# Performance work log

Hardware: AMD Instinct MI355X
Metric: run time of the kernel (lower is better)

Reference implementation:

```python
import jax, jax.numpy as jnp
import numpy as np

IN_DIM = 128
HID = 128
OUT_DIM = 16
DICT_LEN = 400000
N_GATES = 4


def setup_inputs() -> dict:
    key = jax.random.key(0)
    ks = jax.random.split(key, 13)
    s = 0.05  # small init scale (stand-in for orthogonal init)
    return {
        "x_t": jax.random.normal(ks[0], (1, 1, IN_DIM), jnp.float32),
        "h": jax.random.normal(ks[1], (1, 1, HID), jnp.float32) * 0.1,
        "c": jax.random.normal(ks[2], (1, 1, HID), jnp.float32) * 0.1,
        "W_i2h": jax.random.normal(ks[3], ((N_GATES + 1) * HID, IN_DIM), jnp.float32) * s,
        "b_i2h": jnp.zeros(((N_GATES + 1) * HID,), jnp.float32),
        "W_h2h": jax.random.normal(ks[4], ((N_GATES + 1) * HID, HID), jnp.float32) * s,
        "b_h2h": jnp.zeros(((N_GATES + 1) * HID,), jnp.float32),
        "mem_keys": jax.random.normal(ks[5], (DICT_LEN, IN_DIM), jnp.float32),
        "mem_vals": jax.random.normal(ks[6], (DICT_LEN, HID), jnp.float32),
        "W_actor": jax.random.normal(ks[7], (OUT_DIM, HID), jnp.float32) * s,
        "b_actor": jnp.zeros((OUT_DIM,), jnp.float32),
        "W_critic": jax.random.normal(ks[8], (1, HID), jnp.float32) * s,
        "b_critic": jnp.zeros((1,), jnp.float32),
    }


def reference(x_t, h, c, W_i2h, b_i2h, W_h2h, b_h2h, mem_keys, mem_vals,
              W_actor, b_actor, W_critic, b_critic):
    # flatten [1, B, D] -> [B, D] (B == 1)
    x = x_t.reshape(x_t.shape[1], -1)
    hh = h.reshape(h.shape[1], -1)
    cc = c.reshape(c.shape[1], -1)
    hd = hh.shape[-1]

    # fused gate preactivation: i2h(x) + h2h(h), shape [1, 5*H]
    preact = x @ W_i2h.T + b_i2h + hh @ W_h2h.T + b_h2h
    gates = jax.nn.sigmoid(preact[:, :N_GATES * hd])
    f_t = gates[:, :hd]
    i_t = gates[:, hd:2 * hd]
    o_t = gates[:, 2 * hd:3 * hd]
    r_t = gates[:, 3 * hd:4 * hd]
    c_new = jnp.tanh(preact[:, N_GATES * hd:])
    c_t = f_t * cc + i_t * c_new

    # DND read: l2-kernel similarity over all stored keys, softmax-weighted value sum
    d2 = jnp.sum((mem_keys - x) ** 2, axis=-1)          # [L]
    sim = -jnp.sqrt(d2 + 1e-6)                           # F.pairwise_distance eps
    w = jax.nn.softmax(sim)                              # [L]
    m_t = jnp.tanh(w @ mem_vals)[None, :]                # [1, H]

    c_t = c_t + r_t * m_t
    h_t = o_t * jnp.tanh(c_t)

    # A2C heads
    pi = jax.nn.softmax(h_t @ W_actor.T + b_actor, axis=-1)  # [1, OUT]
    v = h_t @ W_critic.T + b_critic                          # [1, 1]

    # DND write: append (key=x_t, val=c_t), drop oldest (fixed-capacity dict)
    keys_new = jnp.concatenate([x, mem_keys[:-1]], axis=0)
    vals_new = jnp.concatenate([c_t, mem_vals[:-1]], axis=0)

    out = jnp.concatenate([pi.ravel(), v.ravel(), h_t.ravel(), c_t.ravel()])
    return out, keys_new, vals_new
```

## Files before the change

kernel.cpp:

```cpp
#include <hip/hip_runtime.h>
#include <hip/hip_bf16.h>
#include <math.h>

#define DICT 400000
#define D 128
#define NPAIR (DICT / 2)
#define G1 1024
#define KEYS_OFF 273
#define VALS_OFF (273 + DICT * D)
#define SHIFT 16.0f

typedef float vfloat4 __attribute__((ext_vector_type(4)));

__global__ __launch_bounds__(256) void k_pre(const float* __restrict__ Wi,
                                             const float* __restrict__ bi,
                                             const float* __restrict__ Wh,
                                             const float* __restrict__ bh,
                                             const float* __restrict__ x,
                                             const float* __restrict__ h,
                                             float* __restrict__ pre) {
    const int lane = threadIdx.x & 63;
    const int row = blockIdx.x * 4 + (threadIdx.x >> 6);
    if (row >= 640) return;
    float2 xv = reinterpret_cast<const float2*>(x)[lane];
    float2 hv = reinterpret_cast<const float2*>(h)[lane];
    float2 wi = reinterpret_cast<const float2*>(Wi + row * D)[lane];
    float2 wh = reinterpret_cast<const float2*>(Wh + row * D)[lane];
    float dot = wi.x * xv.x + wi.y * xv.y + wh.x * hv.x + wh.y * hv.y;
#pragma unroll
    for (int off = 32; off; off >>= 1) dot += __shfl_xor(dot, off);
    if (lane == 0) pre[row] = dot + bi[row] + bh[row];
}

__device__ __forceinline__ void store_window(float* __restrict__ dstK,
                                             float* __restrict__ dstV,
                                             vfloat4 kv, vfloat4 vv,
                                             vfloat4 ek, vfloat4 ev,
                                             int lane, int idx3, int idx4,
                                             int p, bool last) {
    vfloat4 ks, vs;
    float s;
    s = (lane < 3) ? ek.w : kv.w;  ks.x = __shfl(s, idx3);
    s = (lane < 4) ? ek.x : kv.x;  ks.y = __shfl(s, idx4);
    s = (lane < 4) ? ek.y : kv.y;  ks.z = __shfl(s, idx4);
    s = (lane < 4) ? ek.z : kv.z;  ks.w = __shfl(s, idx4);
    s = (lane < 3) ? ev.w : vv.w;  vs.x = __shfl(s, idx3);
    s = (lane < 4) ? ev.x : vv.x;  vs.y = __shfl(s, idx4);
    s = (lane < 4) ? ev.y : vv.y;  vs.z = __shfl(s, idx4);
    s = (lane < 4) ? ev.z : vv.z;  vs.w = __shfl(s, idx4);
    size_t base = (size_t)(2 * p + 1) * 128 + 15 + 4 * (size_t)lane;
    if (!last) {
        *reinterpret_cast<vfloat4*>(dstK + base) = ks;
        *reinterpret_cast<vfloat4*>(dstV + base) = vs;
    } else {
        if (lane < 28) {
            *reinterpret_cast<vfloat4*>(dstK + base) = ks;
            *reinterpret_cast<vfloat4*>(dstV + base) = vs;
        } else if (lane == 28) {
            dstK[base] = ks.x;
            dstV[base] = vs.x;
        }
    }
}

__global__ __launch_bounds__(256) void k_dict(const float* __restrict__ keys,
                                              const float* __restrict__ vals,
                                              const float* __restrict__ x,
                                              float* __restrict__ keys_new,
                                              float* __restrict__ vals_new,
                                              float* __restrict__ partials) {
    const int tid = threadIdx.x;
    const int lane = tid & 63;
    const int half = lane >> 5;
    const int hl = lane & 31;
    const int wv = tid >> 6;
    const int idx3 = (lane + 3) & 63;
    const int idx4 = (lane + 4) & 63;
    const int wave = (blockIdx.x * blockDim.x + tid) >> 6;
    const int nw = (gridDim.x * blockDim.x) >> 6;
    const float4 xv = reinterpret_cast<const float4*>(x)[hl];

    vfloat4 acc = (vfloat4)(0.f);
    float den = 0.f;

#define COMPUTE(kv, vv)                                                             \
    {                                                                               \
        float dx = kv.x - xv.x, dy = kv.y - xv.y, dz = kv.z - xv.z, dw = kv.w - xv.w; \
        float d2 = dx * dx + dy * dy + dz * dz + dw * dw;                           \
        _Pragma("unroll")                                                           \
        for (int off = 16; off; off >>= 1) d2 += __shfl_xor(d2, off);               \
        float e = __expf(SHIFT - sqrtf(d2 + 1e-6f));                                \
        acc.x += e * vv.x; acc.y += e * vv.y;                                       \
        acc.z += e * vv.z; acc.w += e * vv.w;                                       \
        den += e;                                                                   \
    }

    for (int pp = 2 * wave; pp < NPAIR; pp += 2 * nw) {
        const int row0 = 2 * pp + half;
        const int row1 = row0 + 2;
        vfloat4 kv0 = reinterpret_cast<const vfloat4*>(keys + (size_t)row0 * D)[hl];
        vfloat4 kv1 = reinterpret_cast<const vfloat4*>(keys + (size_t)row1 * D)[hl];
        vfloat4 vv0 = reinterpret_cast<const vfloat4*>(vals + (size_t)row0 * D)[hl];
        vfloat4 vv1 = reinterpret_cast<const vfloat4*>(vals + (size_t)row1 * D)[hl];
        vfloat4 ek1 = (vfloat4)(0.f), ev1 = (vfloat4)(0.f);
        if (lane < 4) {
            const int erow = min(2 * pp + 4, DICT - 1);
            ek1 = *reinterpret_cast<const vfloat4*>(keys + (size_t)erow * D + 4 * lane);
            ev1 = *reinterpret_cast<const vfloat4*>(vals + (size_t)erow * D + 4 * lane);
        }

        COMPUTE(kv0, vv0)
        COMPUTE(kv1, vv1)

        if (pp == 0 && lane < 15) {
            keys_new[128 + lane] = keys[lane];
            vals_new[128 + lane] = vals[lane];
        }
        store_window(keys_new, vals_new, kv0, vv0, kv1, vv1, lane, idx3, idx4,
                     pp, false);
        store_window(keys_new, vals_new, kv1, vv1, ek1, ev1, lane, idx3, idx4,
                     pp + 1, pp + 1 == NPAIR - 1);
    }
#undef COMPUTE

    acc.x += __shfl_xor(acc.x, 32);
    acc.y += __shfl_xor(acc.y, 32);
    acc.z += __shfl_xor(acc.z, 32);
    acc.w += __shfl_xor(acc.w, 32);
    den += __shfl_xor(den, 32);

    __shared__ float lnum[4][128];
    __shared__ float lden[4];
    if (lane < 32) {
        lnum[wv][hl * 4 + 0] = acc.x;
        lnum[wv][hl * 4 + 1] = acc.y;
        lnum[wv][hl * 4 + 2] = acc.z;
        lnum[wv][hl * 4 + 3] = acc.w;
    }
    if (lane == 0) lden[wv] = den;
    __syncthreads();
    if (tid < 128) {
        float s = lnum[0][tid] + lnum[1][tid] + lnum[2][tid] + lnum[3][tid];
        partials[(size_t)tid * G1 + blockIdx.x] = s;
    } else if (tid == 128) {
        partials[(size_t)128 * G1 + blockIdx.x] = lden[0] + lden[1] + lden[2] + lden[3];
    }
}

__global__ __launch_bounds__(256) void k_red(const float* __restrict__ partials,
                                             float* __restrict__ red) {
    const int j = blockIdx.x;
    float s = 0.f;
    for (int b = threadIdx.x; b < G1; b += 256) s += partials[(size_t)j * G1 + b];
#pragma unroll
    for (int off = 32; off; off >>= 1) s += __shfl_xor(s, off);
    __shared__ float w4[4];
    if ((threadIdx.x & 63) == 0) w4[threadIdx.x >> 6] = s;
    __syncthreads();
    if (threadIdx.x == 0) red[j] = w4[0] + w4[1] + w4[2] + w4[3];
}

__global__ __launch_bounds__(256) void k_tail(const float* __restrict__ red,
                                              const float* __restrict__ pre,
                                              const float* __restrict__ x,
                                              const float* __restrict__ c,
                                              const float* __restrict__ Wa,
                                              const float* __restrict__ ba,
                                              const float* __restrict__ Wc,
                                              const float* __restrict__ bc,
                                              float* __restrict__ out) {
    __shared__ float sh_h[128];
    __shared__ float sh_logit[16];
    const int tid = threadIdx.x;
    if (tid < 128) {
        float den = red[128];
        float m = tanhf(red[tid] / den);
        float f  = 1.f / (1.f + __expf(-pre[tid]));
        float i_ = 1.f / (1.f + __expf(-pre[128 + tid]));
        float o  = 1.f / (1.f + __expf(-pre[256 + tid]));
        float r  = 1.f / (1.f + __expf(-pre[384 + tid]));
        float cn = tanhf(pre[512 + tid]);
        float ct = f * c[tid] + i_ * cn + r * m;
        float ht = o * tanhf(ct);
        sh_h[tid] = ht;
        out[17 + tid] = ht;
        out[145 + tid] = ct;
        out[KEYS_OFF + tid] = x[tid];
        out[VALS_OFF + tid] = ct;
    }
    __syncthreads();
    if (tid < 16) {
        float l = ba[tid];
        for (int j = 0; j < 128; ++j) l += Wa[tid * D + j] * sh_h[j];
        sh_logit[tid] = l;
    } else if (tid == 16) {
        float v = bc[0];
        for (int j = 0; j < 128; ++j) v += Wc[j] * sh_h[j];
        out[16] = v;
    }
    __syncthreads();
    if (tid == 0) {
        float mx = sh_logit[0];
        for (int k = 1; k < 16; ++k) mx = fmaxf(mx, sh_logit[k]);
        float e[16];
        float s = 0.f;
        for (int k = 0; k < 16; ++k) { e[k] = __expf(sh_logit[k] - mx); s += e[k]; }
        for (int k = 0; k < 16; ++k) out[k] = e[k] / s;
    }
}

extern "C" void kernel_launch(void* const* d_in, const int* in_sizes, int n_in,
                              void* d_out, int out_size, void* d_ws, size_t ws_size,
                              hipStream_t stream) {
    const float* x    = (const float*)d_in[0];
    const float* h    = (const float*)d_in[1];
    const float* c    = (const float*)d_in[2];
    const float* Wi   = (const float*)d_in[3];
    const float* bi   = (const float*)d_in[4];
    const float* Wh   = (const float*)d_in[5];
    const float* bh   = (const float*)d_in[6];
    const float* keys = (const float*)d_in[7];
    const float* vals = (const float*)d_in[8];
    const float* Wa   = (const float*)d_in[9];
    const float* ba   = (const float*)d_in[10];
    const float* Wc   = (const float*)d_in[11];
    const float* bc   = (const float*)d_in[12];
    float* out = (float*)d_out;

    char* ws = (char*)d_ws;
    float* red      = (float*)(ws + 0);
    float* pre      = (float*)(ws + 1024);
    float* partials = (float*)(ws + 4096);

    k_pre<<<160, 256, 0, stream>>>(Wi, bi, Wh, bh, x, h, pre);
    k_dict<<<G1, 256, 0, stream>>>(keys, vals, x, out + KEYS_OFF, out + VALS_OFF, partials);
    k_red<<<129, 256, 0, stream>>>(partials, red);
    k_tail<<<1, 256, 0, stream>>>(red, pre, x, c, Wa, ba, Wc, bc, out);
}
```

Baseline: 183.4 us.

## Split dict pass into key-distance phase and value-accumulate phase via LDS weights

The single fused loop over the dictionary is split into two passes. The first streams keys, computes the softmax weights, stores them in shared memory and writes the shifted keys. The second streams values, reads the cached weights, accumulates the weighted sum and writes the shifted values. This removes the serial dependency where value loads waited behind the distance reduction and cuts register pressure per loop. It relies on each wave doing at most 26 iterations, since the shared weight buffer holds 104 entries per wave, and loop-index bookkeeping is duplicated across the two passes.

```diff
diff --git a/kernel.cpp b/kernel.cpp
--- a/kernel.cpp
+++ b/kernel.cpp
@@ -32,34 +32,22 @@
     if (lane == 0) pre[row] = dot + bi[row] + bh[row];
 }
 
-__device__ __forceinline__ void store_window(float* __restrict__ dstK,
-                                             float* __restrict__ dstV,
-                                             vfloat4 kv, vfloat4 vv,
-                                             vfloat4 ek, vfloat4 ev,
-                                             int lane, int idx3, int idx4,
-                                             int p, bool last) {
-    vfloat4 ks, vs;
+__device__ __forceinline__ void store_window1(float* __restrict__ dst,
+                                              vfloat4 kv, vfloat4 ek,
+                                              int lane, int idx3, int idx4,
+                                              int p, bool last) {
+    vfloat4 ks;
     float s;
     s = (lane < 3) ? ek.w : kv.w;  ks.x = __shfl(s, idx3);
     s = (lane < 4) ? ek.x : kv.x;  ks.y = __shfl(s, idx4);
     s = (lane < 4) ? ek.y : kv.y;  ks.z = __shfl(s, idx4);
     s = (lane < 4) ? ek.z : kv.z;  ks.w = __shfl(s, idx4);
-    s = (lane < 3) ? ev.w : vv.w;  vs.x = __shfl(s, idx3);
-    s = (lane < 4) ? ev.x : vv.x;  vs.y = __shfl(s, idx4);
-    s = (lane < 4) ? ev.y : vv.y;  vs.z = __shfl(s, idx4);
-    s = (lane < 4) ? ev.z : vv.z;  vs.w = __shfl(s, idx4);
     size_t base = (size_t)(2 * p + 1) * 128 + 15 + 4 * (size_t)lane;
     if (!last) {
-        *reinterpret_cast<vfloat4*>(dstK + base) = ks;
-        *reinterpret_cast<vfloat4*>(dstV + base) = vs;
+        *reinterpret_cast<vfloat4*>(dst + base) = ks;
     } else {
-        if (lane < 28) {
-            *reinterpret_cast<vfloat4*>(dstK + base) = ks;
-            *reinterpret_cast<vfloat4*>(dstV + base) = vs;
-        } else if (lane == 28) {
-            dstK[base] = ks.x;
-            dstV[base] = vs.x;
-        }
+        if (lane < 28) *reinterpret_cast<vfloat4*>(dst + base) = ks;
+        else if (lane == 28) dst[base] = ks.x;
     }
 }
 
@@ -80,48 +68,74 @@
     const int nw = (gridDim.x * blockDim.x) >> 6;
     const float4 xv = reinterpret_cast<const float4*>(x)[hl];
 
+    __shared__ float e_lds[4][104];
+
+    float den = 0.f;
+
+    {
+        int it = 0;
+        for (int pp = 2 * wave; pp < NPAIR; pp += 2 * nw, ++it) {
+            const int row0 = 2 * pp + half;
+            const int row1 = row0 + 2;
+            vfloat4 kv0 = reinterpret_cast<const vfloat4*>(keys + (size_t)row0 * D)[hl];
+            vfloat4 kv1 = reinterpret_cast<const vfloat4*>(keys + (size_t)row1 * D)[hl];
+            vfloat4 ek1 = (vfloat4)(0.f);
+            if (lane < 4) {
+                const int erow = min(2 * pp + 4, DICT - 1);
+                ek1 = *reinterpret_cast<const vfloat4*>(keys + (size_t)erow * D + 4 * lane);
+            }
+
+            float dx = kv0.x - xv.x, dy = kv0.y - xv.y, dz = kv0.z - xv.z, dw = kv0.w - xv.w;
+            float d20 = dx * dx + dy * dy + dz * dz + dw * dw;
+            dx = kv1.x - xv.x; dy = kv1.y - xv.y; dz = kv1.z - xv.z; dw = kv1.w - xv.w;
+            float d21 = dx * dx + dy * dy + dz * dz + dw * dw;
+#pragma unroll
+            for (int off = 16; off; off >>= 1) {
+                d20 += __shfl_xor(d20, off);
+                d21 += __shfl_xor(d21, off);
+            }
+            float e0 = __expf(SHIFT - sqrtf(d20 + 1e-6f));
+            float e1 = __expf(SHIFT - sqrtf(d21 + 1e-6f));
+            den += e0 + e1;
+            if (hl == 0) {
+                e_lds[wv][4 * it + 2 * half + 0] = e0;
+                e_lds[wv][4 * it + 2 * half + 1] = e1;
+            }
+
+            if (pp == 0 && lane < 15) keys_new[128 + lane] = keys[lane];
+            store_window1(keys_new, kv0, kv1, lane, idx3, idx4, pp, false);
+            store_window1(keys_new, kv1, ek1, lane, idx3, idx4, pp + 1,
+                          pp + 1 == NPAIR - 1);
+        }
+    }
+
     vfloat4 acc = (vfloat4)(0.f);
-    float den = 0.f;
-
-#define COMPUTE(kv, vv)                                                             \
-    {                                                                               \
-        float dx = kv.x - xv.x, dy = kv.y - xv.y, dz = kv.z - xv.z, dw = kv.w - xv.w; \
-        float d2 = dx * dx + dy * dy + dz * dz + dw * dw;                           \
-        _Pragma("unroll")                                                           \
-        for (int off = 16; off; off >>= 1) d2 += __shfl_xor(d2, off);               \
-        float e = __expf(SHIFT - sqrtf(d2 + 1e-6f));                                \
-        acc.x += e * vv.x; acc.y += e * vv.y;                                       \
-        acc.z += e * vv.z; acc.w += e * vv.w;                                       \
-        den += e;                                                                   \
-    }
-
-    for (int pp = 2 * wave; pp < NPAIR; pp += 2 * nw) {
-        const int row0 = 2 * pp + half;
-        const int row1 = row0 + 2;
-        vfloat4 kv0 = reinterpret_cast<const vfloat4*>(keys + (size_t)row0 * D)[hl];
-        vfloat4 kv1 = reinterpret_cast<const vfloat4*>(keys + (size_t)row1 * D)[hl];
-        vfloat4 vv0 = reinterpret_cast<const vfloat4*>(vals + (size_t)row0 * D)[hl];
-        vfloat4 vv1 = reinterpret_cast<const vfloat4*>(vals + (size_t)row1 * D)[hl];
-        vfloat4 ek1 = (vfloat4)(0.f), ev1 = (vfloat4)(0.f);
-        if (lane < 4) {
-            const int erow = min(2 * pp + 4, DICT - 1);
-            ek1 = *reinterpret_cast<const vfloat4*>(keys + (size_t)erow * D + 4 * lane);
-            ev1 = *reinterpret_cast<const vfloat4*>(vals + (size_t)erow * D + 4 * lane);
+    {
+        int it = 0;
+        for (int pp = 2 * wave; pp < NPAIR; pp += 2 * nw, ++it) {
+            const int row0 = 2 * pp + half;
+            const int row1 = row0 + 2;
+            vfloat4 vv0 = reinterpret_cast<const vfloat4*>(vals + (size_t)row0 * D)[hl];
+            vfloat4 vv1 = reinterpret_cast<const vfloat4*>(vals + (size_t)row1 * D)[hl];
+            vfloat4 ev1 = (vfloat4)(0.f);
+            if (lane < 4) {
+                const int erow = min(2 * pp + 4, DICT - 1);
+                ev1 = *reinterpret_cast<const vfloat4*>(vals + (size_t)erow * D + 4 * lane);
+            }
+
+            float e0 = e_lds[wv][4 * it + 2 * half + 0];
+            float e1 = e_lds[wv][4 * it + 2 * half + 1];
+            acc.x += e0 * vv0.x + e1 * vv1.x;
+            acc.y += e0 * vv0.y + e1 * vv1.y;
+            acc.z += e0 * vv0.z + e1 * vv1.z;
+            acc.w += e0 * vv0.w + e1 * vv1.w;
+
+            if (pp == 0 && lane < 15) vals_new[128 + lane] = vals[lane];
+            store_window1(vals_new, vv0, vv1, lane, idx3, idx4, pp, false);
+            store_window1(vals_new, vv1, ev1, lane, idx3, idx4, pp + 1,
+                          pp + 1 == NPAIR - 1);
         }
-
-        COMPUTE(kv0, vv0)
-        COMPUTE(kv1, vv1)
-
-        if (pp == 0 && lane < 15) {
-            keys_new[128 + lane] = keys[lane];
-            vals_new[128 + lane] = vals[lane];
-        }
-        store_window(keys_new, vals_new, kv0, vv0, kv1, vv1, lane, idx3, idx4,
-                     pp, false);
-        store_window(keys_new, vals_new, kv1, vv1, ek1, ev1, lane, idx3, idx4,
-                     pp + 1, pp + 1 == NPAIR - 1);
-    }
-#undef COMPUTE
+    }
 
     acc.x += __shfl_xor(acc.x, 32);
     acc.y += __shfl_xor(acc.y, 32);
```

Result: faster. 173.2 us (median of 2 runs) (-5.6%).
